# Optimization experiments

Measured on AMD Instinct MI355X. Metric: run time of the kernel, lower is better.

## Reference

```python
import jax, jax.numpy as jnp
import numpy as np

HIDDEN = 768
HEADS = 12
DK = 64
DV = 64

def setup_inputs() -> dict:
    key = jax.random.key(0)
    k1, k2, k3, k4, k5, k6 = jax.random.split(key, 6)
    B, N = 4, 2048
    x = jax.random.normal(k1, (B, HIDDEN, N), dtype=jnp.float32)
    mask = jax.random.randint(k2, (B, N), 0, 2, dtype=jnp.int32)
    # xavier_uniform for Linear(hidden -> d): limit = sqrt(6/(hidden+d))
    def xavier(k, out_d, in_d, lead=()):
        lim = float(np.sqrt(6.0 / (in_d + out_d)))
        return jax.random.uniform(k, lead + (out_d, in_d), jnp.float32, -lim, lim)
    Wq = xavier(k3, DK, HIDDEN, (HEADS,))   # (H, d_k, hidden)
    Wk = xavier(k4, DK, HIDDEN, (HEADS,))
    Wv = xavier(k5, DV, HIDDEN, (HEADS,))
    Wo = xavier(k6, HIDDEN, HEADS * DV)     # (hidden, H*d_v)
    return {"x": x, "Wq": Wq, "Wk": Wk, "Wv": Wv, "Wo": Wo, "mask": mask}

def reference(x, Wq, Wk, Wv, Wo, mask):
    # x: (B, hidden, N) -> (B, N, hidden)
    xt = jnp.transpose(x, (0, 2, 1))
    q = jnp.einsum('bnc,hdc->bhnd', xt, Wq)  # (B,H,N,d_k)
    k = jnp.einsum('bnc,hdc->bhnd', xt, Wk)
    v = jnp.einsum('bnc,hdc->bhnd', xt, Wv)  # (B,H,N,d_v)
    scale = 1.0 / jnp.sqrt(jnp.asarray(DK, x.dtype))
    qk = jnp.einsum('bhnd,bhmd->bhnm', q, k) * scale  # (B,H,N,N)
    neg_inf = jnp.asarray(-jnp.inf, x.dtype)
    qk = jnp.where(mask[:, None, None, :] != 0, qk, neg_inf)  # mask key positions
    attn = jax.nn.softmax(qk, axis=-1)
    ctx = jnp.einsum('bhnm,bhmd->bhnd', attn, v)  # (B,H,N,d_v)
    B, H, N, D = ctx.shape
    combined = jnp.transpose(ctx, (0, 2, 1, 3)).reshape(B, N, H * D)  # cat over heads
    out = jnp.einsum('bnf,cf->bnc', combined, Wo)  # Linear(H*d_v -> hidden)
    return jnp.transpose(out, (0, 2, 1))  # (B, hidden, N)
```

## Files before the change

### kernel.cpp

```cpp
#include <hip/hip_runtime.h>

typedef _Float16 f16;
typedef __attribute__((ext_vector_type(8))) _Float16 f16x8;
typedef __attribute__((ext_vector_type(4))) _Float16 f16x4;
typedef __attribute__((ext_vector_type(4))) float f32x4;

#define DEVINL __device__ __forceinline__

DEVINL void gload16(const void* g, void* l) {
  __builtin_amdgcn_global_load_lds(
      (const __attribute__((address_space(1))) void*)g,
      (__attribute__((address_space(3))) void*)l, 16, 0, 0);
}

DEVINL f32x4 mfma16(f16x8 a, f16x8 b, f32x4 c) {
  return __builtin_amdgcn_mfma_f32_16x16x32_f16(a, b, c, 0, 0, 0);
}

__global__ __launch_bounds__(256) void convert_k(const float* __restrict__ src,
                                                 f16* __restrict__ dst, int n) {
  int i = (blockIdx.x * 256 + threadIdx.x) * 4;
  if (i + 3 < n) {
    f32x4 v = *(const f32x4*)(src + i);
    f16x4 o = {(f16)v[0], (f16)v[1], (f16)v[2], (f16)v[3]};
    *(f16x4*)(dst + i) = o;
  }
}

__global__ __launch_bounds__(256) void transpose_x(const float* __restrict__ x,
                                                   f16* __restrict__ xt) {
  __shared__ __attribute__((aligned(16))) f16 T[64 * 66];
  const int b = blockIdx.z, c0 = blockIdx.y * 64, n0 = blockIdx.x * 64;
  const int t = threadIdx.x;
  const float* xb = x + (size_t)b * 768 * 2048;
#pragma unroll
  for (int r = 0; r < 4; ++r) {
    int chunk = r * 256 + t;
    int row = chunk >> 4, c4 = (chunk & 15) * 4;
    f32x4 v = *(const f32x4*)&xb[(size_t)(c0 + row) * 2048 + n0 + c4];
#pragma unroll
    for (int e = 0; e < 4; ++e) T[row * 66 + c4 + e] = (f16)v[e];
  }
  __syncthreads();
  f16* xtb = xt + (size_t)b * 2048 * 768;
  int n = t >> 2, cp = (t & 3) * 16;
  __attribute__((aligned(16))) f16 vals[16];
#pragma unroll
  for (int j = 0; j < 16; ++j) vals[j] = T[(cp + j) * 66 + n];
  *(f16x8*)&xtb[(size_t)(n0 + n) * 768 + c0 + cp] = *(const f16x8*)&vals[0];
  *(f16x8*)&xtb[(size_t)(n0 + n) * 768 + c0 + cp + 8] = *(const f16x8*)&vals[8];
}

__global__ __launch_bounds__(256, 2)
void gemm_kernel(const f16* __restrict__ A, const f16* __restrict__ Bt,
                 f16* __restrict__ qkt, f16* __restrict__ vbuf,
                 float* __restrict__ outp, int kind) {
  constexpr int K = 768;
  const int b = blockIdx.z;
  const int n0 = blockIdx.x * 128;
  const int m0 = blockIdx.y * 128;
  const int t = threadIdx.x;
  const int lane = t & 63, w = t >> 6, g = lane >> 4, lo = lane & 15;
  const int wm = (w >> 1) * 64, wn = (w & 1) * 64;

  __shared__ __attribute__((aligned(16))) f16 smem[16384];
  f16* As = smem;
  f16* Bs = smem + 8192;

  const f16* Ab = A + (size_t)m0 * K;
  const f16* Bb = Bt + (size_t)b * 2048 * K + (size_t)n0 * K;

  const f32x4 zf = {0.f, 0.f, 0.f, 0.f};
  f32x4 acc[4][4];
#pragma unroll
  for (int i = 0; i < 4; ++i)
#pragma unroll
    for (int j = 0; j < 4; ++j) acc[i][j] = zf;

  for (int kt = 0; kt < K; kt += 64) {
    __syncthreads();
#pragma unroll
    for (int r = 0; r < 4; ++r) {
      int chunk = r * 256 + t;
      int row = chunk >> 3;
      int c8 = (chunk & 7) ^ (row & 7);
      gload16(Ab + (size_t)row * K + kt + c8 * 8, As + chunk * 8);
    }
#pragma unroll
    for (int r = 0; r < 4; ++r) {
      int chunk = r * 256 + t;
      int row = chunk >> 3;
      int c8 = (chunk & 7) ^ (row & 7);
      gload16(Bb + (size_t)row * K + kt + c8 * 8, Bs + chunk * 8);
    }
    __syncthreads();
#pragma unroll
    for (int kk = 0; kk < 2; ++kk) {
      f16x8 af[4], bfr[4];
#pragma unroll
      for (int i = 0; i < 4; ++i) {
        int row = wm + i * 16 + lo;
        af[i] = *(const f16x8*)&As[row * 64 + (((kk * 4 + g) ^ (row & 7)) * 8)];
      }
#pragma unroll
      for (int j = 0; j < 4; ++j) {
        int col = wn + j * 16 + lo;
        bfr[j] = *(const f16x8*)&Bs[col * 64 + (((kk * 4 + g) ^ (col & 7)) * 8)];
      }
#pragma unroll
      for (int i = 0; i < 4; ++i)
#pragma unroll
        for (int j = 0; j < 4; ++j)
          acc[i][j] = mfma16(af[i], bfr[j], acc[i][j]);
    }
  }

  if (kind == 1) {
    float* Cb = outp + (size_t)b * 768 * 2048;
#pragma unroll
    for (int i = 0; i < 4; ++i) {
      int row = m0 + wm + i * 16 + g * 4;
#pragma unroll
      for (int j = 0; j < 4; ++j) {
        int col = n0 + wn + j * 16 + lo;
#pragma unroll
        for (int r2 = 0; r2 < 4; ++r2)
          Cb[(size_t)(row + r2) * 2048 + col] = acc[i][j][r2];
      }
    }
  } else if (m0 >= 1536) {
    f16* Vb = vbuf + (size_t)b * 768 * 2048;
#pragma unroll
    for (int i = 0; i < 4; ++i) {
      int row = m0 - 1536 + wm + i * 16 + g * 4;
#pragma unroll
      for (int j = 0; j < 4; ++j) {
        int col = n0 + wn + j * 16 + lo;
#pragma unroll
        for (int r2 = 0; r2 < 4; ++r2)
          Vb[(size_t)(row + r2) * 2048 + col] = (f16)acc[i][j][r2];
      }
    }
  } else {
    __syncthreads();
    f16* T = smem;
#pragma unroll
    for (int i = 0; i < 4; ++i)
#pragma unroll
      for (int j = 0; j < 4; ++j) {
        int nl = wn + j * 16 + lo;
#pragma unroll
        for (int r2 = 0; r2 < 4; ++r2) {
          int ml = wm + i * 16 + g * 4 + r2;
          T[nl * 128 + (((ml >> 3) ^ (nl & 15)) * 8) + (ml & 7)] =
              (f16)acc[i][j][r2];
        }
      }
    __syncthreads();
    f16* Qb = qkt + (size_t)b * 2048 * 1536;
    int n = t >> 1, half = t & 1;
#pragma unroll
    for (int c = 0; c < 8; ++c) {
      int chunk = half * 8 + c;
      f16x8 v = *(const f16x8*)&T[n * 128 + ((chunk ^ (n & 15)) * 8)];
      *(f16x8*)&Qb[(size_t)(n0 + n) * 1536 + m0 + chunk * 8] = v;
    }
  }
}

__global__ __launch_bounds__(256, 3)
void attn_kernel(const f16* __restrict__ qkt, const f16* __restrict__ vbuf,
                 const int* __restrict__ mask, f16* __restrict__ ctxt) {
  const int bh = blockIdx.y;
  const int b = bh / 12, h = bh % 12;
  const int n0 = blockIdx.x * 128;
  const int t = threadIdx.x;
  const int lane = t & 63, w = t >> 6, g = lane >> 4, lo = lane & 15;

  __shared__ __attribute__((aligned(16))) f16 Kt[8192];
  __shared__ __attribute__((aligned(16))) f16 Vs[8192];
  __shared__ __attribute__((aligned(16))) f16 Ps[8192];
  __shared__ __attribute__((aligned(16))) f16 bias_s[2048];

  const f16* qb = qkt + (size_t)b * 2048 * 1536;
  const int* mb = mask + b * 2048;
#pragma unroll
  for (int r = 0; r < 8; ++r) {
    int i = r * 256 + t;
    bias_s[i] = (f16)(mb[i] ? 0.f : -60000.f);
  }

  constexpr float QS = 0.125f * 1.44269504088896f;
  f16x8 qa[2][2];
#pragma unroll
  for (int fm = 0; fm < 2; ++fm)
#pragma unroll
    for (int kk = 0; kk < 2; ++kk) {
      f16x8 v = *(const f16x8*)&qb[(size_t)(n0 + w * 32 + fm * 16 + lo) * 1536 +
                                   h * 64 + kk * 32 + g * 8];
#pragma unroll
      for (int e = 0; e < 8; ++e) v[e] = (f16)((float)v[e] * QS);
      qa[fm][kk] = v;
    }

  const f32x4 zf = {0.f, 0.f, 0.f, 0.f};
  f32x4 oacc[2][4];
  float mrun[2], lrun[2];
#pragma unroll
  for (int fm = 0; fm < 2; ++fm) {
#pragma unroll
    for (int fd = 0; fd < 4; ++fd) oacc[fm][fd] = zf;
    mrun[fm] = -3e38f;
    lrun[fm] = 0.f;
  }

  const f16* kb_g = qb + 768 + h * 64;
  const f16* vb_g = vbuf + (size_t)b * 768 * 2048 + (size_t)(h * 64) * 2048;
  f16* psw = &Ps[w * 2048];

  for (int mt = 0; mt < 16; ++mt) {
    const int m0 = mt * 128;
    __syncthreads();
#pragma unroll
    for (int r = 0; r < 4; ++r) {
      int chunk = r * 256 + t;
      int row = chunk >> 3;
      int c8 = (chunk & 7) ^ (row & 7);
      gload16(kb_g + (size_t)(m0 + row) * 1536 + c8 * 8, Kt + chunk * 8);
    }
#pragma unroll
    for (int r = 0; r < 4; ++r) {
      int chunk = r * 256 + t;
      int d = chunk >> 4;
      int c16 = (chunk & 15) ^ (d & 15);
      gload16(vb_g + (size_t)d * 2048 + m0 + c16 * 8, Vs + chunk * 8);
    }
    __syncthreads();

    f32x4 sacc[2][8];
#pragma unroll
    for (int fm = 0; fm < 2; ++fm)
#pragma unroll
      for (int fn = 0; fn < 8; ++fn) sacc[fm][fn] = zf;
#pragma unroll
    for (int kk = 0; kk < 2; ++kk)
#pragma unroll
      for (int fn = 0; fn < 8; ++fn) {
        int m = fn * 16 + lo;
        f16x8 kf = *(const f16x8*)&Kt[m * 64 + (((kk * 4 + g) ^ (m & 7)) * 8)];
        sacc[0][fn] = mfma16(kf, qa[0][kk], sacc[0][fn]);
        sacc[1][fn] = mfma16(kf, qa[1][kk], sacc[1][fn]);
      }

#pragma unroll
    for (int fn = 0; fn < 8; ++fn) {
      f16x4 b4 = *(const f16x4*)&bias_s[m0 + fn * 16 + g * 4];
      f32x4 ba = {(float)b4[0], (float)b4[1], (float)b4[2], (float)b4[3]};
      sacc[0][fn] += ba;
      sacc[1][fn] += ba;
    }

    f16x4 p16[2][8];
#pragma unroll
    for (int fm = 0; fm < 2; ++fm) {
      f32x4 vm = sacc[fm][0];
#pragma unroll
      for (int fn = 1; fn < 8; ++fn)
#pragma unroll
        for (int r = 0; r < 4; ++r) vm[r] = fmaxf(vm[r], sacc[fm][fn][r]);
      float mx = fmaxf(fmaxf(vm[0], vm[1]), fmaxf(vm[2], vm[3]));
      mx = fmaxf(mx, __shfl_xor(mx, 16, 64));
      mx = fmaxf(mx, __shfl_xor(mx, 32, 64));
      float mnew = fmaxf(mrun[fm], mx);
      float alpha = __builtin_amdgcn_exp2f(mrun[fm] - mnew);
      mrun[fm] = mnew;
      f32x4 vs_ = zf;
#pragma unroll
      for (int fn = 0; fn < 8; ++fn) {
        f32x4 pv;
#pragma unroll
        for (int r = 0; r < 4; ++r)
          pv[r] = __builtin_amdgcn_exp2f(sacc[fm][fn][r] - mnew);
        vs_ += pv;
        f16x4 ph = {(f16)pv[0], (f16)pv[1], (f16)pv[2], (f16)pv[3]};
        p16[fm][fn] = ph;
      }
      float rs = (vs_[0] + vs_[1]) + (vs_[2] + vs_[3]);
      rs += __shfl_xor(rs, 16, 64);
      rs += __shfl_xor(rs, 32, 64);
      lrun[fm] = lrun[fm] * alpha + rs;
#pragma unroll
      for (int fd = 0; fd < 4; ++fd) oacc[fm][fd] *= alpha;
    }

#pragma unroll
    for (int ph = 0; ph < 2; ++ph) {
#pragma unroll
      for (int fm = 0; fm < 2; ++fm) {
        int q32 = fm * 16 + lo;
        int sw = q32 & 7;
#pragma unroll
        for (int fi = 0; fi < 4; ++fi) {
          int cq = fi * 2 + (g >> 1);
          *(f16x4*)&psw[q32 * 64 + ((cq ^ sw) * 8) + (g & 1) * 4] =
              p16[fm][ph * 4 + fi];
        }
      }
#pragma unroll
      for (int kkl = 0; kkl < 2; ++kkl) {
        int kk = ph * 2 + kkl;
        f16x8 pa[2], vf[4];
#pragma unroll
        for (int fm = 0; fm < 2; ++fm) {
          int q32 = fm * 16 + lo;
          pa[fm] =
              *(const f16x8*)&psw[q32 * 64 + (((kkl * 4 + g) ^ (q32 & 7)) * 8)];
        }
#pragma unroll
        for (int fd = 0; fd < 4; ++fd) {
          int d = fd * 16 + lo;
          vf[fd] = *(const f16x8*)&Vs[d * 128 + (((kk * 4 + g) ^ (d & 15)) * 8)];
        }
#pragma unroll
        for (int fm = 0; fm < 2; ++fm)
#pragma unroll
          for (int fd = 0; fd < 4; ++fd)
            oacc[fm][fd] = mfma16(vf[fd], pa[fm], oacc[fm][fd]);
      }
    }
  }

  __syncthreads();
  f16* T2 = Kt;
#pragma unroll
  for (int fm = 0; fm < 2; ++fm) {
    float rcp = 1.f / lrun[fm];
    int q = w * 32 + fm * 16 + lo;
    int sw = q & 7;
#pragma unroll
    for (int fd = 0; fd < 4; ++fd) {
      int c8 = fd * 2 + (g >> 1);
      f16x4 o4 = {(f16)(oacc[fm][fd][0] * rcp), (f16)(oacc[fm][fd][1] * rcp),
                  (f16)(oacc[fm][fd][2] * rcp), (f16)(oacc[fm][fd][3] * rcp)};
      *(f16x4*)&T2[q * 64 + ((c8 ^ sw) * 8) + (g & 1) * 4] = o4;
    }
  }
  __syncthreads();
  f16* cb = ctxt + (size_t)b * 2048 * 768;
  int qrow = t >> 1, half = t & 1;
#pragma unroll
  for (int c = 0; c < 4; ++c) {
    int c8 = half * 4 + c;
    f16x8 v = *(const f16x8*)&T2[qrow * 64 + ((c8 ^ (qrow & 7)) * 8)];
    *(f16x8*)&cb[(size_t)(n0 + qrow) * 768 + h * 64 + c8 * 8] = v;
  }
}

extern "C" void kernel_launch(void* const* d_in, const int* in_sizes, int n_in,
                              void* d_out, int out_size, void* d_ws,
                              size_t ws_size, hipStream_t stream) {
  const float* x  = (const float*)d_in[0];
  const float* Wq = (const float*)d_in[1];
  const float* Wk = (const float*)d_in[2];
  const float* Wv = (const float*)d_in[3];
  const float* Wo = (const float*)d_in[4];
  const int* mask = (const int*)d_in[5];
  float* out = (float*)d_out;

  f16* Xt   = (f16*)d_ws;
  f16* Wcat = Xt + 6291456;
  f16* Wob  = Wcat + 1769472;
  f16* QKt  = Wob + 589824;
  f16* Vbuf = QKt + 12582912;
  f16* Ctxt = Xt;

  convert_k<<<576, 256, 0, stream>>>(Wq, Wcat, 589824);
  convert_k<<<576, 256, 0, stream>>>(Wk, Wcat + 589824, 589824);
  convert_k<<<576, 256, 0, stream>>>(Wv, Wcat + 1179648, 589824);
  convert_k<<<576, 256, 0, stream>>>(Wo, Wob, 589824);
  transpose_x<<<dim3(32, 12, 4), 256, 0, stream>>>(x, Xt);
  gemm_kernel<<<dim3(16, 18, 4), 256, 0, stream>>>(Wcat, Xt, QKt, Vbuf, nullptr, 0);
  attn_kernel<<<dim3(16, 48), 256, 0, stream>>>(QKt, Vbuf, mask, Ctxt);
  gemm_kernel<<<dim3(16, 6, 4), 256, 0, stream>>>(Wob, Ctxt, nullptr, nullptr, out, 1);
}
```

Before: 259.2 us.

## Double-buffer K/V tiles in attention with 64-key steps; merge QKV weight conversions

The attention kernel now works on 64-key tiles with two K/V shared-memory buffers. The next tile's global-to-LDS loads are issued before computing on the current one, so one barrier per iteration replaces the load-then-sync pattern. The goal is to overlap memory latency with MFMA and softmax work, at the cost of twice as many softmax rescale steps per key range. Separately, the three Q/K/V weight conversion launches become one kernel to cut launch overhead.

```diff
diff --git a/kernel.cpp b/kernel.cpp
--- a/kernel.cpp
+++ b/kernel.cpp
@@ -15,6 +15,18 @@
 
 DEVINL f32x4 mfma16(f16x8 a, f16x8 b, f32x4 c) {
   return __builtin_amdgcn_mfma_f32_16x16x32_f16(a, b, c, 0, 0, 0);
+}
+
+__global__ __launch_bounds__(256) void convert_qkv(const float* __restrict__ wq,
+                                                   const float* __restrict__ wk,
+                                                   const float* __restrict__ wv,
+                                                   f16* __restrict__ dst) {
+  int seg = blockIdx.x / 576;
+  int i = ((blockIdx.x % 576) * 256 + threadIdx.x) * 4;
+  const float* src = seg == 0 ? wq : (seg == 1 ? wk : wv);
+  f32x4 v = *(const f32x4*)(src + i);
+  f16x4 o = {(f16)v[0], (f16)v[1], (f16)v[2], (f16)v[3]};
+  *(f16x4*)(dst + seg * 589824 + i) = o;
 }
 
 __global__ __launch_bounds__(256) void convert_k(const float* __restrict__ src,
@@ -177,9 +189,9 @@
   const int t = threadIdx.x;
   const int lane = t & 63, w = t >> 6, g = lane >> 4, lo = lane & 15;
 
-  __shared__ __attribute__((aligned(16))) f16 Kt[8192];
-  __shared__ __attribute__((aligned(16))) f16 Vs[8192];
-  __shared__ __attribute__((aligned(16))) f16 Ps[8192];
+  __shared__ __attribute__((aligned(16))) f16 Kd[2][4096];
+  __shared__ __attribute__((aligned(16))) f16 Vd[2][4096];
+  __shared__ __attribute__((aligned(16))) f16 Ps[4][2048];
   __shared__ __attribute__((aligned(16))) f16 bias_s[2048];
 
   const f16* qb = qkt + (size_t)b * 2048 * 1536;
@@ -216,56 +228,65 @@
 
   const f16* kb_g = qb + 768 + h * 64;
   const f16* vb_g = vbuf + (size_t)b * 768 * 2048 + (size_t)(h * 64) * 2048;
-  f16* psw = &Ps[w * 2048];
-
-  for (int mt = 0; mt < 16; ++mt) {
-    const int m0 = mt * 128;
-    __syncthreads();
-#pragma unroll
-    for (int r = 0; r < 4; ++r) {
-      int chunk = r * 256 + t;
-      int row = chunk >> 3;
-      int c8 = (chunk & 7) ^ (row & 7);
-      gload16(kb_g + (size_t)(m0 + row) * 1536 + c8 * 8, Kt + chunk * 8);
-    }
-#pragma unroll
-    for (int r = 0; r < 4; ++r) {
-      int chunk = r * 256 + t;
-      int d = chunk >> 4;
-      int c16 = (chunk & 15) ^ (d & 15);
-      gload16(vb_g + (size_t)d * 2048 + m0 + c16 * 8, Vs + chunk * 8);
-    }
-    __syncthreads();
-
-    f32x4 sacc[2][8];
+  f16* psw = &Ps[w][0];
+
+#define STAGE_KV(BUF, M0)                                                     \
+  {                                                                           \
+    _Pragma("unroll") for (int r = 0; r < 2; ++r) {                           \
+      int chunk = r * 256 + t;                                                \
+      int row = chunk >> 3;                                                   \
+      int c8 = (chunk & 7) ^ (row & 7);                                       \
+      gload16(kb_g + (size_t)((M0) + row) * 1536 + c8 * 8,                    \
+              &Kd[BUF][0] + chunk * 8);                                       \
+    }                                                                         \
+    _Pragma("unroll") for (int r = 0; r < 2; ++r) {                           \
+      int chunk = r * 256 + t;                                                \
+      int d = chunk >> 3;                                                     \
+      int c8 = (chunk & 7) ^ (d & 7);                                         \
+      gload16(vb_g + (size_t)d * 2048 + (M0) + c8 * 8, &Vd[BUF][0] + chunk * 8);\
+    }                                                                         \
+  }
+
+  STAGE_KV(0, 0);
+  __syncthreads();
+
+  for (int mt = 0; mt < 32; ++mt) {
+    const int cur = mt & 1;
+    const int m0 = mt * 64;
+    if (mt + 1 < 32) STAGE_KV(cur ^ 1, m0 + 64);
+
+    const f16* Kb = &Kd[cur][0];
+    const f16* Vb = &Vd[cur][0];
+
+    f32x4 sacc[2][4];
 #pragma unroll
     for (int fm = 0; fm < 2; ++fm)
 #pragma unroll
-      for (int fn = 0; fn < 8; ++fn) sacc[fm][fn] = zf;
+      for (int fn = 0; fn < 4; ++fn) sacc[fm][fn] = zf;
 #pragma unroll
     for (int kk = 0; kk < 2; ++kk)
 #pragma unroll
-      for (int fn = 0; fn < 8; ++fn) {
+      for (int fn = 0; fn < 4; ++fn) {
         int m = fn * 16 + lo;
-        f16x8 kf = *(const f16x8*)&Kt[m * 64 + (((kk * 4 + g) ^ (m & 7)) * 8)];
+        f16x8 kf = *(const f16x8*)&Kb[m * 64 + (((kk * 4 + g) ^ (m & 7)) * 8)];
         sacc[0][fn] = mfma16(kf, qa[0][kk], sacc[0][fn]);
         sacc[1][fn] = mfma16(kf, qa[1][kk], sacc[1][fn]);
       }
 
 #pragma unroll
-    for (int fn = 0; fn < 8; ++fn) {
+    for (int fn = 0; fn < 4; ++fn) {
       f16x4 b4 = *(const f16x4*)&bias_s[m0 + fn * 16 + g * 4];
       f32x4 ba = {(float)b4[0], (float)b4[1], (float)b4[2], (float)b4[3]};
       sacc[0][fn] += ba;
       sacc[1][fn] += ba;
     }
 
-    f16x4 p16[2][8];
+    f16x4 p16[2][4];
 #pragma unroll
     for (int fm = 0; fm < 2; ++fm) {
       f32x4 vm = sacc[fm][0];
 #pragma unroll
-      for (int fn = 1; fn < 8; ++fn)
+      for (int fn = 1; fn < 4; ++fn)
 #pragma unroll
         for (int r = 0; r < 4; ++r) vm[r] = fmaxf(vm[r], sacc[fm][fn][r]);
       float mx = fmaxf(fmaxf(vm[0], vm[1]), fmaxf(vm[2], vm[3]));
@@ -276,7 +297,7 @@
       mrun[fm] = mnew;
       f32x4 vs_ = zf;
 #pragma unroll
-      for (int fn = 0; fn < 8; ++fn) {
+      for (int fn = 0; fn < 4; ++fn) {
         f32x4 pv;
 #pragma unroll
         for (int r = 0; r < 4; ++r)
@@ -294,44 +315,40 @@
     }
 
 #pragma unroll
-    for (int ph = 0; ph < 2; ++ph) {
+    for (int fm = 0; fm < 2; ++fm) {
+      int q32 = fm * 16 + lo;
+      int sw = q32 & 7;
+#pragma unroll
+      for (int fn = 0; fn < 4; ++fn) {
+        int cq = fn * 2 + (g >> 1);
+        *(f16x4*)&psw[q32 * 64 + ((cq ^ sw) * 8) + (g & 1) * 4] = p16[fm][fn];
+      }
+    }
+#pragma unroll
+    for (int kk = 0; kk < 2; ++kk) {
+      f16x8 pa[2], vf[4];
 #pragma unroll
       for (int fm = 0; fm < 2; ++fm) {
         int q32 = fm * 16 + lo;
-        int sw = q32 & 7;
-#pragma unroll
-        for (int fi = 0; fi < 4; ++fi) {
-          int cq = fi * 2 + (g >> 1);
-          *(f16x4*)&psw[q32 * 64 + ((cq ^ sw) * 8) + (g & 1) * 4] =
-              p16[fm][ph * 4 + fi];
-        }
-      }
-#pragma unroll
-      for (int kkl = 0; kkl < 2; ++kkl) {
-        int kk = ph * 2 + kkl;
-        f16x8 pa[2], vf[4];
-#pragma unroll
-        for (int fm = 0; fm < 2; ++fm) {
-          int q32 = fm * 16 + lo;
-          pa[fm] =
-              *(const f16x8*)&psw[q32 * 64 + (((kkl * 4 + g) ^ (q32 & 7)) * 8)];
-        }
-#pragma unroll
-        for (int fd = 0; fd < 4; ++fd) {
-          int d = fd * 16 + lo;
-          vf[fd] = *(const f16x8*)&Vs[d * 128 + (((kk * 4 + g) ^ (d & 15)) * 8)];
-        }
-#pragma unroll
-        for (int fm = 0; fm < 2; ++fm)
-#pragma unroll
-          for (int fd = 0; fd < 4; ++fd)
-            oacc[fm][fd] = mfma16(vf[fd], pa[fm], oacc[fm][fd]);
-      }
-    }
-  }
-
-  __syncthreads();
-  f16* T2 = Kt;
+        pa[fm] =
+            *(const f16x8*)&psw[q32 * 64 + (((kk * 4 + g) ^ (q32 & 7)) * 8)];
+      }
+#pragma unroll
+      for (int fd = 0; fd < 4; ++fd) {
+        int d = fd * 16 + lo;
+        vf[fd] = *(const f16x8*)&Vb[d * 64 + (((kk * 4 + g) ^ (d & 7)) * 8)];
+      }
+#pragma unroll
+      for (int fm = 0; fm < 2; ++fm)
+#pragma unroll
+        for (int fd = 0; fd < 4; ++fd)
+          oacc[fm][fd] = mfma16(vf[fd], pa[fm], oacc[fm][fd]);
+    }
+
+    __syncthreads();
+  }
+
+  f16* T2 = &Kd[0][0];
 #pragma unroll
   for (int fm = 0; fm < 2; ++fm) {
     float rcp = 1.f / lrun[fm];
@@ -354,6 +371,7 @@
     f16x8 v = *(const f16x8*)&T2[qrow * 64 + ((c8 ^ (qrow & 7)) * 8)];
     *(f16x8*)&cb[(size_t)(n0 + qrow) * 768 + h * 64 + c8 * 8] = v;
   }
+#undef STAGE_KV
 }
 
 extern "C" void kernel_launch(void* const* d_in, const int* in_sizes, int n_in,
@@ -374,9 +392,7 @@
   f16* Vbuf = QKt + 12582912;
   f16* Ctxt = Xt;
 
-  convert_k<<<576, 256, 0, stream>>>(Wq, Wcat, 589824);
-  convert_k<<<576, 256, 0, stream>>>(Wk, Wcat + 589824, 589824);
-  convert_k<<<576, 256, 0, stream>>>(Wv, Wcat + 1179648, 589824);
+  convert_qkv<<<1728, 256, 0, stream>>>(Wq, Wk, Wv, Wcat);
   convert_k<<<576, 256, 0, stream>>>(Wo, Wob, 589824);
   transpose_x<<<dim3(32, 12, 4), 256, 0, stream>>>(x, Xt);
   gemm_kernel<<<dim3(16, 18, 4), 256, 0, stream>>>(Wcat, Xt, QKt, Vbuf, nullptr, 0);
```

Result: faster. 237.7 us (-8.3%).
